# Kernel optimization log

Hardware: AMD Instinct MI355X
Metric: run time of the kernel (lower is better)

## Reference

```python
import jax, jax.numpy as jnp
import numpy as np

N = 262144   # number of units (batched instances of the module)
G = 128      # universe_field side length
D = 128      # dimension
RADIUS = 3   # min(3, G//2) == 3

# First D=128 neighborhood offsets in the original triple-loop order (i-major, j, k)
_grid = np.stack(np.meshgrid(np.arange(-RADIUS, RADIUS + 1),
                             np.arange(-RADIUS, RADIUS + 1),
                             np.arange(-RADIUS, RADIUS + 1), indexing='ij'), -1).reshape(-1, 3)[:D]
OI = jnp.asarray(_grid[:, 0], dtype=jnp.int32)
OJ = jnp.asarray(_grid[:, 1], dtype=jnp.int32)
OK = jnp.asarray(_grid[:, 2], dtype=jnp.int32)


def setup_inputs() -> dict:
    key = jax.random.key(0)
    ks = jax.random.split(key, 8)
    return {
        'universe_field': jax.random.normal(ks[0], (G, G, G), jnp.float32),
        'positions': jax.random.uniform(ks[1], (N, 3), jnp.float32) * G,
        'signatures': jax.random.normal(ks[2], (N, D), jnp.float32),
        'offsets': jax.random.normal(ks[3], (N, 3), jnp.float32) * 0.1,
        'W1': jax.random.normal(ks[4], (2 * D, D), jnp.float32) * (1.0 / np.sqrt(2 * D)),
        'b1': jax.random.normal(ks[5], (D,), jnp.float32) * 0.01,
        'W2': jax.random.normal(ks[6], (D, D), jnp.float32) * (1.0 / np.sqrt(D)),
        'b2': jax.random.normal(ks[7], (D,), jnp.float32) * 0.01,
    }


def _sample_local(field, pos):
    # pos: [N,3] float; truncate to int (torch .long()) then clamp, like the original
    pc = jnp.clip(jax.lax.stop_gradient(pos).astype(jnp.int32), 0, G - 1)  # [N,3]
    xx = jnp.clip(pc[:, 0:1] + OI[None, :], 0, G - 1)  # [N,D]
    yy = jnp.clip(pc[:, 1:2] + OJ[None, :], 0, G - 1)
    zz = jnp.clip(pc[:, 2:3] + OK[None, :], 0, G - 1)
    return field[xx, yy, zz]  # [N,D] gathered local field (343 points truncated to D)


def _stability(field, pos, signatures, W1, b1, W2, b2):
    local = _sample_local(field, pos)                       # [N,D]
    combined = jnp.concatenate([signatures, local], axis=-1)  # [N,2D]
    h = jnp.tanh(combined @ W1 + b1)                        # [N,D]
    resp = h @ W2 + b2                                      # [N,D]
    return jnp.linalg.norm(resp - signatures, axis=-1)      # [N]


def reference(universe_field, positions, signatures, offsets, W1, b1, W2, b2):
    stab_old = _stability(universe_field, positions, signatures, W1, b1, W2, b2)
    test_pos = positions + offsets
    stab_new = _stability(universe_field, test_pos, signatures, W1, b1, W2, b2)
    accept = stab_new <= stab_old                           # revert move if new_stab > old_stab
    final_pos = jnp.where(accept[:, None], test_pos, positions)
    stability = jnp.where(accept, stab_new, stab_old)
    return stability, final_pos
```

## Files before the change

kernel.cpp:

```cpp
#include <hip/hip_runtime.h>
#include <hip/hip_bf16.h>

#define NU 262144
#define GG 128
#define PG 134
#define DD 128

typedef __attribute__((ext_vector_type(8))) short short8;
typedef __attribute__((ext_vector_type(4))) float f32x4;

union Frag { short8 s; unsigned u[4]; };

__device__ __forceinline__ unsigned short f2b(float f) {
  union { float f; unsigned u; } v; v.f = f;
  unsigned r = v.u + 0x7fffu + ((v.u >> 16) & 1u);
  return (unsigned short)(r >> 16);
}
__device__ __forceinline__ unsigned cvtpk(float lo, float hi) {
  unsigned r;
  asm("v_cvt_pk_bf16_f32 %0, %1, %2" : "=v"(r) : "v"(lo), "v"(hi));
  return r;
}
__device__ __forceinline__ float unplo(unsigned w) {
  union { unsigned u; float f; } v; v.u = w << 16; return v.f;
}
__device__ __forceinline__ float unphi(unsigned w) {
  union { unsigned u; float f; } v; v.u = w & 0xffff0000u; return v.f;
}

__device__ __forceinline__ float fast_tanh(float x) {
  float e = __expf(fabsf(x) * 2.0f);
  float r = __frcp_rn(e + 1.0f);
  return copysignf(fmaf(-2.0f, r, 1.0f), x);
}

struct alignas(16) RowdT { int v[20]; };
static constexpr RowdT mkrowd() {
  RowdT t{};
  for (int r = 0; r < 20; ++r) {
    int rr = (r < 18) ? r : 18;
    int di = (rr < 18) ? (-3 + rr / 7) : -1;
    int dj = (rr < 18) ? (-3 + rr % 7) : 1;
    t.v[r] = (di * PG + dj) * PG - 3;
  }
  return t;
}
__device__ constexpr RowdT ROWD = mkrowd();

__global__ void prep_field(const float* __restrict__ f, unsigned short* __restrict__ fp) {
  int idx = blockIdx.x * 256 + threadIdx.x;
  if (idx >= PG * PG * PG) return;
  int z = idx % PG, t = idx / PG;
  int y = t % PG, x = t / PG;
  int xx = min(max(x - 3, 0), GG - 1);
  int yy = min(max(y - 3, 0), GG - 1);
  int zz = min(max(z - 3, 0), GG - 1);
  fp[idx] = f2b(f[(xx * GG + yy) * GG + zz]);
}

__global__ void prep_w(const float* __restrict__ W1, const float* __restrict__ W2,
                       unsigned short* __restrict__ wall) {
  int idx = blockIdx.x * 256 + threadIdx.x;
  if (idx >= 6656) return;
  int kt = idx >> 9, nt = (idx >> 6) & 7, ln = idx & 63;
  int n = nt * 16 + (ln & 15), lg = ln >> 4;
  short8 s;
  if (kt < 4) {
    int k0 = kt * 32 + lg * 8;
#pragma unroll
    for (int j = 0; j < 8; ++j) s[j] = (short)f2b(W1[(k0 + j) * DD + n]);
  } else if (kt < 9) {
    int r = (kt - 4) * 4 + lg;
#pragma unroll
    for (int j = 0; j < 8; ++j) {
      bool valid = (r < 18 && j < 7) || (r == 18 && j < 2);
      int row = 128 + ((r < 18) ? (r * 7 + j) : (126 + j));
      s[j] = valid ? (short)f2b(W1[row * DD + n]) : (short)0;
    }
  } else {
    int k0 = (kt - 9) * 32 + lg * 8;
#pragma unroll
    for (int j = 0; j < 8; ++j) s[j] = (short)f2b(W2[(k0 + j) * DD + n]);
  }
  ((short8*)wall)[idx] = s;
}

__global__ __launch_bounds__(512, 4) void atu_main(
    const float* __restrict__ pos, const float* __restrict__ sig,
    const float* __restrict__ offs,
    const float* __restrict__ b1, const float* __restrict__ b2,
    const unsigned short* __restrict__ fpad, const unsigned short* __restrict__ wall,
    float* __restrict__ out_stab, float* __restrict__ out_pos)
{
  __shared__ unsigned short ldsw[2][8192];
  __shared__ alignas(16) unsigned short ns[8][2048];
  const int tid  = threadIdx.x;
  const int lane = tid & 63;
  const int lg   = lane >> 4, lm = lane & 15;
  const int wid  = tid >> 6;
  int bid = blockIdx.x;
  int swz = (bid & 7) * 256 + (bid >> 3);
  const int ub = swz * 128 + wid * 16;
  const int un = ub + lm;
  char* nsb = (char*)&ns[wid][0];
  const char* wallb = (const char*)wall;
  const char* fpadb = (const char*)fpad;

  int abase[2];
  {
    float px = pos[un * 3 + 0], py = pos[un * 3 + 1], pz = pos[un * 3 + 2];
    float qx = px + offs[un * 3 + 0], qy = py + offs[un * 3 + 1], qz = pz + offs[un * 3 + 2];
    int ax = min(max((int)px, 0), GG - 1), ay = min(max((int)py, 0), GG - 1), az = min(max((int)pz, 0), GG - 1);
    int bx = min(max((int)qx, 0), GG - 1), by = min(max((int)qy, 0), GG - 1), bz = min(max((int)qz, 0), GG - 1);
    abase[0] = ((ax + 3) * PG + (ay + 3)) * PG + (az + 3);
    abase[1] = ((bx + 3) * PG + (by + 3)) * PG + (bz + 3);
  }

#define GLL2(KTA, H)                                                              \
  __builtin_amdgcn_global_load_lds(                                               \
      (const unsigned*)(wallb + (((KTA) * 512 + tid) * 16)),                      \
      (unsigned*)((char*)&ldsw[H][0] + wid * 1024), 16, 0, 0);                    \
  __builtin_amdgcn_global_load_lds(                                               \
      (const unsigned*)(wallb + ((((KTA) + 1) * 512 + tid) * 16)),                \
      (unsigned*)((char*)&ldsw[H][0] + 8192 + wid * 1024), 16, 0, 0);

#define GLL1(KTA, H)                                                              \
  __builtin_amdgcn_global_load_lds(                                               \
      (const unsigned*)(wallb + (((KTA) * 512 + tid) * 16)),                      \
      (unsigned*)((char*)&ldsw[H][0] + wid * 1024), 16, 0, 0);

  GLL2(0, 0)
  f32x4 spa = *(const f32x4*)(sig + (size_t)un * DD + lg * 8);
  f32x4 spb = *(const f32x4*)(sig + (size_t)un * DD + lg * 8 + 4);
  short8 rAc, rBc;
  {
    int rd = ROWD.v[lg];
    rAc = *(const short8*)(fpadb + 2 * (size_t)(abase[0] + rd));
    rBc = *(const short8*)(fpadb + 2 * (size_t)(abase[1] + rd));
  }

  f32x4 acc[8][2];
#pragma unroll
  for (int nt = 0; nt < 8; ++nt) acc[nt][0] = *(const f32x4*)(b1 + nt * 16 + lg * 4);
  f32x4 acc2[8][2];
  unsigned Q[2][8][2];

  __syncthreads();

#define SIG_KT(KT, HALF)                                                          \
  {                                                                               \
    f32x4 na, nb;                                                                 \
    if ((KT) < 3) {                                                               \
      na = *(const f32x4*)(sig + (size_t)un * DD + ((KT) + 1) * 32 + lg * 8);     \
      nb = *(const f32x4*)(sig + (size_t)un * DD + ((KT) + 1) * 32 + lg * 8 + 4); \
    }                                                                             \
    Frag B;                                                                       \
    B.u[0] = cvtpk(spa[0], spa[1]); B.u[1] = cvtpk(spa[2], spa[3]);               \
    B.u[2] = cvtpk(spb[0], spb[1]); B.u[3] = cvtpk(spb[2], spb[3]);               \
    *(short8*)(nsb + ((KT) * 4 + lg) * 256 + lm * 16) = B.s;                      \
    const char* buf = (const char*)&ldsw[HALF][0] + (((KT) & 1) ? 8192 : 0);      \
    _Pragma("unroll")                                                             \
    for (int nt = 0; nt < 8; ++nt) {                                              \
      short8 af = *(const short8*)(buf + (nt * 64 + lane) * 16);                  \
      acc[nt][0] = __builtin_amdgcn_mfma_f32_16x16x32_bf16(af, B.s, acc[nt][0], 0, 0, 0); \
    }                                                                             \
    if ((KT) < 3) { spa = na; spb = nb; }                                         \
  }

#define ROW_KT(KT, HALF)                                                          \
  {                                                                               \
    short8 nA, nB;                                                                \
    if ((KT) < 8) {                                                               \
      int rn = ROWD.v[((KT) - 3) * 4 + lg];                                       \
      nA = *(const short8*)(fpadb + 2 * (size_t)(abase[0] + rn));                 \
      nB = *(const short8*)(fpadb + 2 * (size_t)(abase[1] + rn));                 \
    }                                                                             \
    const char* buf = (const char*)&ldsw[HALF][0] + (((KT) & 1) ? 8192 : 0);      \
    _Pragma("unroll")                                                             \
    for (int nt = 0; nt < 8; ++nt) {                                              \
      short8 af = *(const short8*)(buf + (nt * 64 + lane) * 16);                  \
      acc[nt][0] = __builtin_amdgcn_mfma_f32_16x16x32_bf16(af, rAc, acc[nt][0], 0, 0, 0); \
      acc[nt][1] = __builtin_amdgcn_mfma_f32_16x16x32_bf16(af, rBc, acc[nt][1], 0, 0, 0); \
    }                                                                             \
    if ((KT) < 8) { rAc = nA; rBc = nB; }                                         \
  }

#define G2_KT(KT, HALF)                                                           \
  {                                                                               \
    constexpr int kb = (KT) - 9;                                                  \
    Frag W[2];                                                                    \
    _Pragma("unroll")                                                             \
    for (int ut = 0; ut < 2; ++ut) {                                              \
      int qa0 = (int)Q[ut][2 * kb][0],     qa1 = (int)Q[ut][2 * kb][1];           \
      int qb0 = (int)Q[ut][2 * kb + 1][0], qb1 = (int)Q[ut][2 * kb + 1][1];       \
      int r00 = __builtin_amdgcn_ds_bpermute(ad0, qa0);                           \
      int r01 = __builtin_amdgcn_ds_bpermute(ad0, qa1);                           \
      int r10 = __builtin_amdgcn_ds_bpermute(ad1, qa0);                           \
      int r11 = __builtin_amdgcn_ds_bpermute(ad1, qa1);                           \
      int s00 = __builtin_amdgcn_ds_bpermute(ad0, qb0);                           \
      int s01 = __builtin_amdgcn_ds_bpermute(ad0, qb1);                           \
      int s10 = __builtin_amdgcn_ds_bpermute(ad1, qb0);                           \
      int s11 = __builtin_amdgcn_ds_bpermute(ad1, qb1);                           \
      W[ut].u[0] = (unsigned)(hi ? s00 : r00);                                    \
      W[ut].u[1] = (unsigned)(hi ? s01 : r01);                                    \
      W[ut].u[2] = (unsigned)(hi ? s10 : r10);                                    \
      W[ut].u[3] = (unsigned)(hi ? s11 : r11);                                    \
    }                                                                             \
    const char* buf = (const char*)&ldsw[HALF][0] + (((KT) & 1) ? 8192 : 0);      \
    _Pragma("unroll")                                                             \
    for (int nt = 0; nt < 8; ++nt) {                                              \
      short8 af = *(const short8*)(buf + (nt * 64 + lane) * 16);                  \
      acc2[nt][0] = __builtin_amdgcn_mfma_f32_16x16x32_bf16(af, W[0].s, acc2[nt][0], 0, 0, 0); \
      acc2[nt][1] = __builtin_amdgcn_mfma_f32_16x16x32_bf16(af, W[1].s, acc2[nt][1], 0, 0, 0); \
    }                                                                             \
  }

  const int ad0 = ((((2 * lg) & 3) * 16) + lm) * 4;
  const int ad1 = ((((2 * lg + 1) & 3) * 16) + lm) * 4;
  const bool hi = (lg >= 2);

  GLL2(2, 1)
  SIG_KT(0, 0) SIG_KT(1, 0)
  __syncthreads();

  GLL2(4, 0)
  SIG_KT(2, 1) SIG_KT(3, 1)
  __syncthreads();

#pragma unroll
  for (int nt = 0; nt < 8; ++nt) acc[nt][1] = acc[nt][0];

  GLL2(6, 1)
  ROW_KT(4, 0) ROW_KT(5, 0)
  __syncthreads();

  GLL2(8, 0)
  ROW_KT(6, 1) ROW_KT(7, 1)
  __syncthreads();

  GLL2(10, 1)
  ROW_KT(8, 0)

#pragma unroll
  for (int nt = 0; nt < 8; ++nt) {
#pragma unroll
    for (int ut = 0; ut < 2; ++ut) {
      float h0 = fast_tanh(acc[nt][ut][0]);
      float h1 = fast_tanh(acc[nt][ut][1]);
      float h2 = fast_tanh(acc[nt][ut][2]);
      float h3 = fast_tanh(acc[nt][ut][3]);
      Q[ut][nt][0] = cvtpk(h0, h1);
      Q[ut][nt][1] = cvtpk(h2, h3);
    }
  }
#pragma unroll
  for (int nt = 0; nt < 8; ++nt) {
    f32x4 b2v = *(const f32x4*)(b2 + nt * 16 + lg * 4);
    acc2[nt][0] = b2v; acc2[nt][1] = b2v;
  }

  G2_KT(9, 0)
  __syncthreads();

  GLL1(12, 0)
  G2_KT(10, 1) G2_KT(11, 1)
  __syncthreads();

  G2_KT(12, 0)

  float ssq[2] = {0.f, 0.f};
#pragma unroll
  for (int nt = 0; nt < 8; ++nt) {
    unsigned long long w64 = *(const unsigned long long*)
        (nsb + (nt * 2 + (lg >> 1)) * 256 + lm * 16 + (lg & 1) * 8);
    unsigned w0 = (unsigned)w64, w1 = (unsigned)(w64 >> 32);
    float sv0 = unplo(w0), sv1 = unphi(w0);
    float sv2 = unplo(w1), sv3 = unphi(w1);
#pragma unroll
    for (int ut = 0; ut < 2; ++ut) {
      float d0 = acc2[nt][ut][0] - sv0;
      float d1 = acc2[nt][ut][1] - sv1;
      float d2 = acc2[nt][ut][2] - sv2;
      float d3 = acc2[nt][ut][3] - sv3;
      ssq[ut] = fmaf(d0, d0, ssq[ut]);
      ssq[ut] = fmaf(d1, d1, ssq[ut]);
      ssq[ut] = fmaf(d2, d2, ssq[ut]);
      ssq[ut] = fmaf(d3, d3, ssq[ut]);
    }
  }
  ssq[0] += __shfl_xor(ssq[0], 16, 64); ssq[0] += __shfl_xor(ssq[0], 32, 64);
  ssq[1] += __shfl_xor(ssq[1], 16, 64); ssq[1] += __shfl_xor(ssq[1], 32, 64);

  if (lane < 16) {
    float px = pos[un * 3 + 0], py = pos[un * 3 + 1], pz = pos[un * 3 + 2];
    float ox = offs[un * 3 + 0], oy = offs[un * 3 + 1], oz = offs[un * 3 + 2];
    bool ok = ssq[1] <= ssq[0];
    out_stab[un] = sqrtf(ok ? ssq[1] : ssq[0]);
    out_pos[un * 3 + 0] = ok ? px + ox : px;
    out_pos[un * 3 + 1] = ok ? py + oy : py;
    out_pos[un * 3 + 2] = ok ? pz + oz : pz;
  }
#undef GLL2
#undef GLL1
#undef SIG_KT
#undef ROW_KT
#undef G2_KT
}

extern "C" void kernel_launch(void* const* d_in, const int* in_sizes, int n_in,
                              void* d_out, int out_size, void* d_ws, size_t ws_size,
                              hipStream_t stream) {
  const float* field = (const float*)d_in[0];
  const float* pos   = (const float*)d_in[1];
  const float* sig   = (const float*)d_in[2];
  const float* offs  = (const float*)d_in[3];
  const float* W1    = (const float*)d_in[4];
  const float* b1    = (const float*)d_in[5];
  const float* W2    = (const float*)d_in[6];
  const float* b2    = (const float*)d_in[7];
  float* out_stab = (float*)d_out;
  float* out_pos  = out_stab + NU;

  char* ws = (char*)d_ws;
  unsigned short* fpad = (unsigned short*)ws;
  unsigned short* wall = (unsigned short*)(ws + 4812800);

  prep_field<<<(PG * PG * PG + 255) / 256, 256, 0, stream>>>(field, fpad);
  prep_w<<<26, 256, 0, stream>>>(W1, W2, wall);
  atu_main<<<NU / 128, 512, 0, stream>>>(pos, sig, offs, b1, b2,
                                         fpad, wall, out_stab, out_pos);
}
```

Before: 137.3 us.

## Preload all weights into LDS once per 1024-thread block, drop per-stage barriers

Each block now has 16 waves and 256 units, and loads the full bf16 W1/W2 tile set (~104 KB) into dynamic LDS in a single upfront step. This replaces the double-buffered per-k-tile staging and the barriers between stages. The bf16 signature copy used in the residual is rebuilt from global loads into registers instead of being stored in LDS. The aim is less barrier stalling and weight reloads per unit, at the cost of much larger LDS per block, one block per CU, and more registers and global signature reads.

```diff
diff --git a/kernel.cpp b/kernel.cpp
--- a/kernel.cpp
+++ b/kernel.cpp
@@ -85,26 +85,34 @@
   ((short8*)wall)[idx] = s;
 }
 
-__global__ __launch_bounds__(512, 4) void atu_main(
+__global__ __launch_bounds__(1024, 1) void atu_main(
     const float* __restrict__ pos, const float* __restrict__ sig,
     const float* __restrict__ offs,
     const float* __restrict__ b1, const float* __restrict__ b2,
     const unsigned short* __restrict__ fpad, const unsigned short* __restrict__ wall,
     float* __restrict__ out_stab, float* __restrict__ out_pos)
 {
-  __shared__ unsigned short ldsw[2][8192];
-  __shared__ alignas(16) unsigned short ns[8][2048];
+  extern __shared__ char ldsraw[];
   const int tid  = threadIdx.x;
   const int lane = tid & 63;
   const int lg   = lane >> 4, lm = lane & 15;
   const int wid  = tid >> 6;
   int bid = blockIdx.x;
-  int swz = (bid & 7) * 256 + (bid >> 3);
-  const int ub = swz * 128 + wid * 16;
+  int swz = (bid & 7) * 128 + (bid >> 3);
+  const int ub = swz * 256 + wid * 16;
   const int un = ub + lm;
-  char* nsb = (char*)&ns[wid][0];
   const char* wallb = (const char*)wall;
   const char* fpadb = (const char*)fpad;
+
+#pragma unroll
+  for (int i = 0; i < 7; ++i) {
+    int fb = i * 1024 + (wid << 6);
+    if (fb < 6656) {
+      __builtin_amdgcn_global_load_lds(
+          (const unsigned*)(wallb + (size_t)(fb + lane) * 16),
+          (unsigned*)(ldsraw + (size_t)fb * 16), 16, 0, 0);
+    }
+  }
 
   int abase[2];
   {
@@ -116,20 +124,6 @@
     abase[1] = ((bx + 3) * PG + (by + 3)) * PG + (bz + 3);
   }
 
-#define GLL2(KTA, H)                                                              \
-  __builtin_amdgcn_global_load_lds(                                               \
-      (const unsigned*)(wallb + (((KTA) * 512 + tid) * 16)),                      \
-      (unsigned*)((char*)&ldsw[H][0] + wid * 1024), 16, 0, 0);                    \
-  __builtin_amdgcn_global_load_lds(                                               \
-      (const unsigned*)(wallb + ((((KTA) + 1) * 512 + tid) * 16)),                \
-      (unsigned*)((char*)&ldsw[H][0] + 8192 + wid * 1024), 16, 0, 0);
-
-#define GLL1(KTA, H)                                                              \
-  __builtin_amdgcn_global_load_lds(                                               \
-      (const unsigned*)(wallb + (((KTA) * 512 + tid) * 16)),                      \
-      (unsigned*)((char*)&ldsw[H][0] + wid * 1024), 16, 0, 0);
-
-  GLL2(0, 0)
   f32x4 spa = *(const f32x4*)(sig + (size_t)un * DD + lg * 8);
   f32x4 spb = *(const f32x4*)(sig + (size_t)un * DD + lg * 8 + 4);
   short8 rAc, rBc;
@@ -144,21 +138,30 @@
   for (int nt = 0; nt < 8; ++nt) acc[nt][0] = *(const f32x4*)(b1 + nt * 16 + lg * 4);
   f32x4 acc2[8][2];
   unsigned Q[2][8][2];
+  unsigned nsv[8][2];
 
   __syncthreads();
 
-#define SIG_KT(KT, HALF)                                                          \
+#define SIG_KT(KT)                                                                \
   {                                                                               \
     f32x4 na, nb;                                                                 \
     if ((KT) < 3) {                                                               \
       na = *(const f32x4*)(sig + (size_t)un * DD + ((KT) + 1) * 32 + lg * 8);     \
       nb = *(const f32x4*)(sig + (size_t)un * DD + ((KT) + 1) * 32 + lg * 8 + 4); \
     }                                                                             \
+        \
+    {                                                                             \
+      f32x4 nv0 = *(const f32x4*)(sig + (size_t)un * DD + (2 * (KT)) * 16 + lg * 4);     \
+      f32x4 nv1 = *(const f32x4*)(sig + (size_t)un * DD + (2 * (KT) + 1) * 16 + lg * 4); \
+      nsv[2 * (KT)][0]     = cvtpk(nv0[0], nv0[1]);                               \
+      nsv[2 * (KT)][1]     = cvtpk(nv0[2], nv0[3]);                               \
+      nsv[2 * (KT) + 1][0] = cvtpk(nv1[0], nv1[1]);                               \
+      nsv[2 * (KT) + 1][1] = cvtpk(nv1[2], nv1[3]);                               \
+    }                                                                             \
     Frag B;                                                                       \
     B.u[0] = cvtpk(spa[0], spa[1]); B.u[1] = cvtpk(spa[2], spa[3]);               \
     B.u[2] = cvtpk(spb[0], spb[1]); B.u[3] = cvtpk(spb[2], spb[3]);               \
-    *(short8*)(nsb + ((KT) * 4 + lg) * 256 + lm * 16) = B.s;                      \
-    const char* buf = (const char*)&ldsw[HALF][0] + (((KT) & 1) ? 8192 : 0);      \
+    const char* buf = ldsraw + (KT) * 8192;                                       \
     _Pragma("unroll")                                                             \
     for (int nt = 0; nt < 8; ++nt) {                                              \
       short8 af = *(const short8*)(buf + (nt * 64 + lane) * 16);                  \
@@ -167,7 +170,7 @@
     if ((KT) < 3) { spa = na; spb = nb; }                                         \
   }
 
-#define ROW_KT(KT, HALF)                                                          \
+#define ROW_KT(KT)                                                                \
   {                                                                               \
     short8 nA, nB;                                                                \
     if ((KT) < 8) {                                                               \
@@ -175,7 +178,7 @@
       nA = *(const short8*)(fpadb + 2 * (size_t)(abase[0] + rn));                 \
       nB = *(const short8*)(fpadb + 2 * (size_t)(abase[1] + rn));                 \
     }                                                                             \
-    const char* buf = (const char*)&ldsw[HALF][0] + (((KT) & 1) ? 8192 : 0);      \
+    const char* buf = ldsraw + (KT) * 8192;                                       \
     _Pragma("unroll")                                                             \
     for (int nt = 0; nt < 8; ++nt) {                                              \
       short8 af = *(const short8*)(buf + (nt * 64 + lane) * 16);                  \
@@ -185,7 +188,7 @@
     if ((KT) < 8) { rAc = nA; rBc = nB; }                                         \
   }
 
-#define G2_KT(KT, HALF)                                                           \
+#define G2_KT(KT)                                                                 \
   {                                                                               \
     constexpr int kb = (KT) - 9;                                                  \
     Frag W[2];                                                                    \
@@ -206,7 +209,7 @@
       W[ut].u[2] = (unsigned)(hi ? s10 : r10);                                    \
       W[ut].u[3] = (unsigned)(hi ? s11 : r11);                                    \
     }                                                                             \
-    const char* buf = (const char*)&ldsw[HALF][0] + (((KT) & 1) ? 8192 : 0);      \
+    const char* buf = ldsraw + (KT) * 8192;                                       \
     _Pragma("unroll")                                                             \
     for (int nt = 0; nt < 8; ++nt) {                                              \
       short8 af = *(const short8*)(buf + (nt * 64 + lane) * 16);                  \
@@ -219,27 +222,12 @@
   const int ad1 = ((((2 * lg + 1) & 3) * 16) + lm) * 4;
   const bool hi = (lg >= 2);
 
-  GLL2(2, 1)
-  SIG_KT(0, 0) SIG_KT(1, 0)
-  __syncthreads();
-
-  GLL2(4, 0)
-  SIG_KT(2, 1) SIG_KT(3, 1)
-  __syncthreads();
+  SIG_KT(0) SIG_KT(1) SIG_KT(2) SIG_KT(3)
 
 #pragma unroll
   for (int nt = 0; nt < 8; ++nt) acc[nt][1] = acc[nt][0];
 
-  GLL2(6, 1)
-  ROW_KT(4, 0) ROW_KT(5, 0)
-  __syncthreads();
-
-  GLL2(8, 0)
-  ROW_KT(6, 1) ROW_KT(7, 1)
-  __syncthreads();
-
-  GLL2(10, 1)
-  ROW_KT(8, 0)
+  ROW_KT(4) ROW_KT(5) ROW_KT(6) ROW_KT(7) ROW_KT(8)
 
 #pragma unroll
   for (int nt = 0; nt < 8; ++nt) {
@@ -259,23 +247,13 @@
     acc2[nt][0] = b2v; acc2[nt][1] = b2v;
   }
 
-  G2_KT(9, 0)
-  __syncthreads();
-
-  GLL1(12, 0)
-  G2_KT(10, 1) G2_KT(11, 1)
-  __syncthreads();
-
-  G2_KT(12, 0)
+  G2_KT(9) G2_KT(10) G2_KT(11) G2_KT(12)
 
   float ssq[2] = {0.f, 0.f};
 #pragma unroll
   for (int nt = 0; nt < 8; ++nt) {
-    unsigned long long w64 = *(const unsigned long long*)
-        (nsb + (nt * 2 + (lg >> 1)) * 256 + lm * 16 + (lg & 1) * 8);
-    unsigned w0 = (unsigned)w64, w1 = (unsigned)(w64 >> 32);
-    float sv0 = unplo(w0), sv1 = unphi(w0);
-    float sv2 = unplo(w1), sv3 = unphi(w1);
+    float sv0 = unplo(nsv[nt][0]), sv1 = unphi(nsv[nt][0]);
+    float sv2 = unplo(nsv[nt][1]), sv3 = unphi(nsv[nt][1]);
 #pragma unroll
     for (int ut = 0; ut < 2; ++ut) {
       float d0 = acc2[nt][ut][0] - sv0;
@@ -300,8 +278,6 @@
     out_pos[un * 3 + 1] = ok ? py + oy : py;
     out_pos[un * 3 + 2] = ok ? pz + oz : pz;
   }
-#undef GLL2
-#undef GLL1
 #undef SIG_KT
 #undef ROW_KT
 #undef G2_KT
@@ -327,6 +303,6 @@
 
   prep_field<<<(PG * PG * PG + 255) / 256, 256, 0, stream>>>(field, fpad);
   prep_w<<<26, 256, 0, stream>>>(W1, W2, wall);
-  atu_main<<<NU / 128, 512, 0, stream>>>(pos, sig, offs, b1, b2,
-                                         fpad, wall, out_stab, out_pos);
-}
+  atu_main<<<NU / 256, 1024, 106496, stream>>>(pos, sig, offs, b1, b2,
+                                               fpad, wall, out_stab, out_pos);
+}
```

Result: slower. 157.3 us (+14.6%).
